# Kernel optimization log

Hardware: AMD Instinct MI355X
Metric: run time of the kernel (lower is better)

Reference implementation:

```python
import jax, jax.numpy as jnp
import numpy as np

NUM_NODES = 100000
NUM_EDGES = 600000
NUM_GRAPHS = 512
D = 128  # num_features == latent widths


def setup_inputs() -> dict:
    key = jax.random.key(0)
    ks = jax.random.split(key, 16)
    inp = {
        "x": jax.random.normal(ks[0], (NUM_NODES, D), dtype=jnp.float32),
        "edge_index": jax.random.randint(ks[1], (2, NUM_EDGES), 0, NUM_NODES, dtype=jnp.int32),
        "batch": jnp.sort(jax.random.randint(ks[2], (NUM_NODES,), 0, NUM_GRAPHS, dtype=jnp.int32)),
    }
    s = 1.0 / np.sqrt(D)
    # SAGEConv params per layer: lin_l (applied to mean-aggregated neighbors), lin_r (root), bias
    for i in range(3):
        inp[f"Wl{i+1}"] = jax.random.uniform(ks[3 + 3 * i], (D, D), jnp.float32, -s, s)
        inp[f"Wr{i+1}"] = jax.random.uniform(ks[4 + 3 * i], (D, D), jnp.float32, -s, s)
        inp[f"b{i+1}"] = jax.random.uniform(ks[5 + 3 * i], (D,), jnp.float32, -s, s)
    inp["Wro"] = jax.random.uniform(ks[12], (D, 1), jnp.float32, -s, s)
    inp["bro"] = jax.random.uniform(ks[13], (1,), jnp.float32, -s, s)
    return inp


def _sage_conv(h, Wl, Wr, b, src, dst):
    # mean aggregation of source features at destination nodes
    msg = jax.ops.segment_sum(h[src], dst, num_segments=NUM_NODES)          # [N, D]
    cnt = jax.ops.segment_sum(jnp.ones((src.shape[0], 1), h.dtype), dst,
                              num_segments=NUM_NODES)                        # [N, 1]
    mean = msg / jnp.maximum(cnt, 1.0)
    return mean @ Wl + h @ Wr + b


def reference(x, edge_index, batch, Wl1, Wr1, b1, Wl2, Wr2, b2, Wl3, Wr3, b3, Wro, bro):
    src, dst = edge_index[0], edge_index[1]
    h = x
    for Wl, Wr, b in ((Wl1, Wr1, b1), (Wl2, Wr2, b2), (Wl3, Wr3, b3)):
        h = jax.nn.relu(_sage_conv(h, Wl, Wr, b, src, dst))
    # per-graph sum pooling (replaces the python loop over unique batch ids)
    pooled = jax.ops.segment_sum(h, batch, num_segments=NUM_GRAPHS)  # [G, D]
    return jax.nn.sigmoid(pooled @ Wro + bro)  # [G, 1]
```

## Files before the change

### kernel.cpp

```cpp
#include <hip/hip_runtime.h>
#include <math.h>

#define N_NODES 100000
#define N_EDGES 600000
#define N_GRAPHS 512
#define D 128
#define SCAN_BS 1024
#define SCAN_NBC ((N_NODES + SCAN_BS - 1) / SCAN_BS)

typedef unsigned short u16;
typedef __attribute__((ext_vector_type(8))) short short8;
typedef __attribute__((ext_vector_type(4))) float f32x4;

__device__ __forceinline__ u16 f2bf(float f) {
    unsigned int u = __float_as_uint(f);
    u += 0x7FFFu + ((u >> 16) & 1u);
    return (u16)(u >> 16);
}
__device__ __forceinline__ float bf2f(u16 h) {
    return __uint_as_float(((unsigned int)h) << 16);
}
__device__ __forceinline__ void split2(float f, unsigned int& h16, unsigned int& l16) {
    unsigned int u = __float_as_uint(f);
    unsigned int hb = (u + (0x7FFFu + ((u >> 16) & 1u))) & 0xffff0000u;
    float lo = f - __uint_as_float(hb);
    unsigned int ul = __float_as_uint(lo);
    h16 = hb >> 16;
    l16 = (ul + (0x7FFFu + ((ul >> 16) & 1u))) >> 16;
}

typedef __attribute__((address_space(1))) const unsigned int gas_u32;
typedef __attribute__((address_space(3))) unsigned int las_u32;
__device__ __forceinline__ void gload16(const void* g, void* l) {
    __builtin_amdgcn_global_load_lds((gas_u32*)g, (las_u32*)l, 16, 0, 0);
}

__global__ __launch_bounds__(256) void zero_i_kernel(int* __restrict__ p, int n) {
    int i = blockIdx.x * 256 + threadIdx.x;
    if (i < n) p[i] = 0;
}

__global__ __launch_bounds__(256) void hist_kernel(const int* __restrict__ dst,
                                                   int* __restrict__ deg) {
    int e = blockIdx.x * 256 + threadIdx.x;
    if (e < N_EDGES) atomicAdd(&deg[dst[e]], 1);
}

__global__ __launch_bounds__(1024) void scan1_kernel(const int* __restrict__ deg,
                                                     int* __restrict__ excl,
                                                     int* __restrict__ blocksum) {
    __shared__ int buf[2][SCAN_BS];
    const int t = threadIdx.x;
    const int gid = blockIdx.x * SCAN_BS + t;
    int v = (gid < N_NODES) ? deg[gid] : 0;
    buf[0][t] = v;
    __syncthreads();
    int pi = 0;
    for (int off = 1; off < SCAN_BS; off <<= 1) {
        int val = buf[pi][t];
        if (t >= off) val += buf[pi][t - off];
        buf[pi ^ 1][t] = val;
        pi ^= 1;
        __syncthreads();
    }
    int incl = buf[pi][t];
    if (gid < N_NODES) excl[gid] = incl - v;
    if (t == SCAN_BS - 1) blocksum[blockIdx.x] = incl;
}

__global__ __launch_bounds__(256) void scan3_kernel(const int* __restrict__ excl,
                                                    const int* __restrict__ blocksum,
                                                    int* __restrict__ rowptr) {
    __shared__ int buf[2][128];
    const int t = threadIdx.x;
    if (t < 128) buf[0][t] = (t < SCAN_NBC) ? blocksum[t] : 0;
    __syncthreads();
    int pi = 0;
    for (int off = 1; off < 128; off <<= 1) {
        if (t < 128) {
            int val = buf[pi][t];
            if (t >= off) val += buf[pi][t - off];
            buf[pi ^ 1][t] = val;
        }
        pi ^= 1;
        __syncthreads();
    }
    const int i = blockIdx.x * 256 + t;
    if (i < N_NODES) {
        const int j = i / SCAN_BS;
        const int pref = (j == 0) ? 0 : buf[pi][j - 1];
        rowptr[i] = excl[i] + pref;
    }
    if (i == 0) rowptr[N_NODES] = N_EDGES;
}

__global__ __launch_bounds__(256) void fill_kernel(const int* __restrict__ src,
                                                   const int* __restrict__ dst,
                                                   const int* __restrict__ rowptr,
                                                   int* __restrict__ fill,
                                                   int* __restrict__ csr_src) {
    int e = blockIdx.x * 256 + threadIdx.x;
    if (e < N_EDGES) {
        int d = dst[e];
        int pos = rowptr[d] + atomicAdd(&fill[d], 1);
        csr_src[pos] = src[e];
    }
}

__global__ __launch_bounds__(256) void split_x_kernel(const float* __restrict__ x,
                                                      u16* __restrict__ Hhi,
                                                      u16* __restrict__ Hlo) {
    const int i = blockIdx.x * 256 + threadIdx.x;
    const float4 v = ((const float4*)x)[i];
    unsigned int h0, l0, h1, l1, h2, l2, h3, l3;
    split2(v.x, h0, l0); split2(v.y, h1, l1);
    split2(v.z, h2, l2); split2(v.w, h3, l3);
    uint2 oh, ol;
    oh.x = h0 | (h1 << 16); oh.y = h2 | (h3 << 16);
    ol.x = l0 | (l1 << 16); ol.y = l2 | (l3 << 16);
    ((uint2*)Hhi)[i] = oh;
    ((uint2*)Hlo)[i] = ol;
}

__global__ __launch_bounds__(64) void wprep_kernel(const float* __restrict__ Wl1, const float* __restrict__ Wr1,
                                                   const float* __restrict__ Wl2, const float* __restrict__ Wr2,
                                                   const float* __restrict__ Wl3, const float* __restrict__ Wr3,
                                                   u16* __restrict__ wph, u16* __restrict__ wpl) {
    const int layer = blockIdx.x >> 6;
    const int t = blockIdx.x & 63;
    const int lane = threadIdx.x;
    const float* Wl = (layer == 0) ? Wl1 : (layer == 1) ? Wl2 : Wl3;
    const float* Wr = (layer == 0) ? Wr1 : (layer == 1) ? Wr2 : Wr3;
    const int nt = t >> 3, kt = t & 7;
    const int n = nt * 16 + (lane & 15);
    const int k0 = kt * 32 + (lane >> 4) * 8;
    const size_t base = (size_t)layer * 32768 + (size_t)(t * 64 + lane) * 8;
    #pragma unroll
    for (int j = 0; j < 8; ++j) {
        const int k = k0 + j;
        const float w = (k < 128) ? Wl[k * 128 + n] : Wr[(k - 128) * 128 + n];
        const u16 h = f2bf(w);
        wph[base + j] = h;
        wpl[base + j] = f2bf(w - bf2f(h));
    }
}

__global__ __launch_bounds__(256) void agg_kernel(const u16* __restrict__ Hhi,
                                                  const int* __restrict__ rowptr,
                                                  const int* __restrict__ csr_src,
                                                  u16* __restrict__ Mb) {
    const int lane = threadIdx.x & 63;
    const int node = blockIdx.x * 4 + (threadIdx.x >> 6);
    if (node >= N_NODES) return;
    const int beg = rowptr[node];
    const int end = rowptr[node + 1];
    const unsigned int* H32 = (const unsigned int*)Hhi;
    float a0 = 0.f, a1 = 0.f;

    for (int c0 = beg; c0 < end; c0 += 64) {
        const int nv = min(64, end - c0);
        int msrc = (c0 + lane < end) ? csr_src[c0 + lane] : 0;
        int j = 0;
        for (; j + 4 <= nv; j += 4) {
            const int s0 = __shfl(msrc, j + 0);
            const int s1 = __shfl(msrc, j + 1);
            const int s2 = __shfl(msrc, j + 2);
            const int s3 = __shfl(msrc, j + 3);
            const unsigned int w0 = H32[(size_t)s0 * 64 + lane];
            const unsigned int w1 = H32[(size_t)s1 * 64 + lane];
            const unsigned int w2 = H32[(size_t)s2 * 64 + lane];
            const unsigned int w3 = H32[(size_t)s3 * 64 + lane];
            a0 += __uint_as_float(w0 << 16) + __uint_as_float(w1 << 16)
                + __uint_as_float(w2 << 16) + __uint_as_float(w3 << 16);
            a1 += __uint_as_float(w0 & 0xffff0000u) + __uint_as_float(w1 & 0xffff0000u)
                + __uint_as_float(w2 & 0xffff0000u) + __uint_as_float(w3 & 0xffff0000u);
        }
        for (; j < nv; ++j) {
            const int s = __shfl(msrc, j);
            const unsigned int w = H32[(size_t)s * 64 + lane];
            a0 += __uint_as_float(w << 16);
            a1 += __uint_as_float(w & 0xffff0000u);
        }
    }
    const float inv = 1.0f / (float)max(end - beg, 1);
    const unsigned int o = (unsigned int)f2bf(a0 * inv) | ((unsigned int)f2bf(a1 * inv) << 16);
    ((unsigned int*)Mb)[(size_t)node * 64 + lane] = o;
}

__global__ __launch_bounds__(512, 4) void gemm_kernel(const u16* __restrict__ Mb,
                                                      const u16* Hhi, const u16* Hlo,
                                                      const u16* __restrict__ Wph,
                                                      const u16* __restrict__ Wpl,
                                                      const float* __restrict__ bias,
                                                      u16* OHhi, u16* OHlo,
                                                      const float* __restrict__ Wro,
                                                      float* rowdot) {
    __shared__ uint4 ldsAll[5120];
    const int t = threadIdx.x;
    const int lane = t & 63;
    const int wv = t >> 6;
    const int m0 = blockIdx.x * 128 + wv * 16;
    int rm = m0 + (lane & 15);
    if (rm >= N_NODES) rm = 0;
    const int ko = (lane >> 4) * 8;

    short8 am[4], ah[4], al[4];
    #pragma unroll
    for (int kt = 0; kt < 4; ++kt) {
        am[kt] = *(const short8*)(Mb  + (size_t)rm * D + kt * 32 + ko);
        ah[kt] = *(const short8*)(Hhi + (size_t)rm * D + kt * 32 + ko);
        al[kt] = *(const short8*)(Hlo + (size_t)rm * D + kt * 32 + ko);
    }

    const int rowb = m0 + ((lane >> 4) << 2);
    const int cl = lane & 15;
    const int g4 = (lane >> 4) << 2;
    const u16* ldsU = (const u16*)ldsAll;
    char* bounceB = (char*)ldsAll + 65536 + wv * 2048;
    float wsum[4] = {0.f, 0.f, 0.f, 0.f};

    #pragma unroll
    for (int s = 0; s < 2; ++s) {
        if (s) __syncthreads();
        {
            const uint4* gh = (const uint4*)Wph + s * 2048;
            const uint4* gl = (const uint4*)Wpl + s * 2048;
            #pragma unroll
            for (int i = 0; i < 4; ++i) {
                gload16(gh + t + 512 * i, (void*)&ldsAll[wv * 64 + 512 * i]);
                gload16(gl + t + 512 * i, (void*)&ldsAll[2048 + wv * 64 + 512 * i]);
            }
        }
        __syncthreads();

        f32x4 acc4[4];
        #pragma unroll
        for (int nt2 = 0; nt2 < 4; ++nt2) {
            f32x4 acc = {0.f, 0.f, 0.f, 0.f};
            #pragma unroll
            for (int kt = 0; kt < 8; ++kt) {
                const int fo = (nt2 * 8 + kt) * 512 + lane * 8;
                const short8 bh = *(const short8*)(ldsU + fo);
                const short8 bl = *(const short8*)(ldsU + 16384 + fo);
                if (kt < 4) {
                    acc = __builtin_amdgcn_mfma_f32_16x16x32_bf16(am[kt], bh, acc, 0, 0, 0);
                    acc = __builtin_amdgcn_mfma_f32_16x16x32_bf16(am[kt], bl, acc, 0, 0, 0);
                } else {
                    acc = __builtin_amdgcn_mfma_f32_16x16x32_bf16(ah[kt - 4], bh, acc, 0, 0, 0);
                    acc = __builtin_amdgcn_mfma_f32_16x16x32_bf16(ah[kt - 4], bl, acc, 0, 0, 0);
                    acc = __builtin_amdgcn_mfma_f32_16x16x32_bf16(al[kt - 4], bh, acc, 0, 0, 0);
                }
            }
            acc4[nt2] = acc;
        }

        if (rowdot) {
            #pragma unroll
            for (int nt2 = 0; nt2 < 4; ++nt2) {
                const int col = (s * 4 + nt2) * 16 + cl;
                const float bv = bias[col];
                const float wroc = Wro[col];
                #pragma unroll
                for (int r = 0; r < 4; ++r) {
                    const float v = fmaxf(acc4[nt2][r] + bv, 0.f);
                    wsum[r] = fmaf(v, wroc, wsum[r]);
                }
            }
        } else {
            unsigned int lo_pack[8];
            #pragma unroll
            for (int nt2 = 0; nt2 < 4; ++nt2) {
                const int col = (s * 4 + nt2) * 16 + cl;
                const float bv = bias[col];
                #pragma unroll
                for (int r = 0; r < 4; ++r) {
                    const int row16 = g4 + r;
                    const float v = fmaxf(acc4[nt2][r] + bv, 0.f);
                    unsigned int h16, l16;
                    split2(v, h16, l16);
                    const int boff = (row16 * 128 + (nt2 * 16 + cl) * 2) ^ ((row16 & 7) << 4);
                    *(u16*)(bounceB + boff) = (u16)h16;
                    if (r & 1) lo_pack[nt2 * 2 + (r >> 1)] |= l16 << 16;
                    else       lo_pack[nt2 * 2 + (r >> 1)]  = l16;
                }
            }
            asm volatile("s_waitcnt lgkmcnt(0)" ::: "memory");
            #pragma unroll
            for (int j = 0; j < 2; ++j) {
                const int row16 = j * 8 + (lane >> 3);
                const int blk = lane & 7;
                const uint4 vv = *(const uint4*)(bounceB + row16 * 128 + ((blk ^ (row16 & 7)) << 4));
                const int grow = blockIdx.x * 128 + wv * 16 + row16;
                if (grow < N_NODES)
                    *(uint4*)(OHhi + (size_t)grow * D + s * 64 + blk * 8) = vv;
            }
            asm volatile("s_waitcnt lgkmcnt(0)" ::: "memory");
            #pragma unroll
            for (int nt2 = 0; nt2 < 4; ++nt2) {
                #pragma unroll
                for (int r = 0; r < 4; ++r) {
                    const int row16 = g4 + r;
                    const unsigned int l16 = (lo_pack[nt2 * 2 + (r >> 1)] >> ((r & 1) * 16)) & 0xffffu;
                    const int boff = (row16 * 128 + (nt2 * 16 + cl) * 2) ^ ((row16 & 7) << 4);
                    *(u16*)(bounceB + boff) = (u16)l16;
                }
            }
            asm volatile("s_waitcnt lgkmcnt(0)" ::: "memory");
            #pragma unroll
            for (int j = 0; j < 2; ++j) {
                const int row16 = j * 8 + (lane >> 3);
                const int blk = lane & 7;
                const uint4 vv = *(const uint4*)(bounceB + row16 * 128 + ((blk ^ (row16 & 7)) << 4));
                const int grow = blockIdx.x * 128 + wv * 16 + row16;
                if (grow < N_NODES)
                    *(uint4*)(OHlo + (size_t)grow * D + s * 64 + blk * 8) = vv;
            }
        }
    }

    if (rowdot) {
        #pragma unroll
        for (int r = 0; r < 4; ++r) {
            float tsum = wsum[r];
            tsum += __shfl_down(tsum, 8, 64);
            tsum += __shfl_down(tsum, 4, 64);
            tsum += __shfl_down(tsum, 2, 64);
            tsum += __shfl_down(tsum, 1, 64);
            const int row = rowb + r;
            if (cl == 0 && row < N_NODES) {
                rowdot[row] = tsum;
            }
        }
    }
}

__global__ __launch_bounds__(64) void final_kernel(const float* __restrict__ rowdot,
                                                   const int* __restrict__ batch,
                                                   const float* __restrict__ bro,
                                                   float* __restrict__ out) {
    const int g = blockIdx.x;
    const int t = threadIdx.x;
    int lo = 0, hi = N_NODES;
    while (lo < hi) { int mid = (lo + hi) >> 1; if (batch[mid] < g) lo = mid + 1; else hi = mid; }
    int lo2 = lo, hi2 = N_NODES;
    while (lo2 < hi2) { int mid = (lo2 + hi2) >> 1; if (batch[mid] < g + 1) lo2 = mid + 1; else hi2 = mid; }

    float acc = 0.0f;
    for (int i = lo + t; i < lo2; i += 64) acc += rowdot[i];
    #pragma unroll
    for (int off = 32; off > 0; off >>= 1) acc += __shfl_down(acc, off, 64);
    if (t == 0) out[g] = 1.0f / (1.0f + expf(-(acc + bro[0])));
}

extern "C" void kernel_launch(void* const* d_in, const int* in_sizes, int n_in,
                              void* d_out, int out_size, void* d_ws, size_t ws_size,
                              hipStream_t stream) {
    const float* x     = (const float*)d_in[0];
    const int*   ei    = (const int*)d_in[1];
    const int*   batch = (const int*)d_in[2];
    const int*   src   = ei;
    const int*   dst   = ei + N_EDGES;
    const float* Wl[3] = {(const float*)d_in[3], (const float*)d_in[6], (const float*)d_in[9]};
    const float* Wr[3] = {(const float*)d_in[4], (const float*)d_in[7], (const float*)d_in[10]};
    const float* bs[3] = {(const float*)d_in[5], (const float*)d_in[8], (const float*)d_in[11]};
    const float* Wro   = (const float*)d_in[12];
    const float* bro   = (const float*)d_in[13];
    float* out = (float*)d_out;

    const size_t ND = (size_t)N_NODES * D;
    char* ws = (char*)d_ws;
    u16* Hhi = (u16*)ws;
    u16* Hlo = Hhi + ND;
    u16* Mb  = Hlo + ND;
    u16* Wph = Mb + ND;
    u16* Wpl = Wph + 3 * 32768;
    int* deg      = (int*)(Wpl + 3 * 32768);
    int* fill     = deg + N_NODES;
    float* rowdot = (float*)(fill + N_NODES);
    int* excl     = (int*)(rowdot + N_NODES);
    int* blocksum = excl + N_NODES;
    int* rowptr   = blocksum + 128;
    int* csr_src  = rowptr + N_NODES + 1;

    const int EB      = (N_EDGES + 255) / 256;
    const int NB      = (N_NODES + 255) / 256;
    const int NB2     = (2 * N_NODES + 255) / 256;
    const int SPLIT_B = (int)(ND / 4 / 256);
    const int AGG_B   = N_NODES / 4;
    const int GEMM_B  = (N_NODES + 127) / 128;

    zero_i_kernel<<<NB2, 256, 0, stream>>>(deg, 2 * N_NODES);
    hist_kernel<<<EB, 256, 0, stream>>>(dst, deg);
    scan1_kernel<<<SCAN_NBC, SCAN_BS, 0, stream>>>(deg, excl, blocksum);
    scan3_kernel<<<NB, 256, 0, stream>>>(excl, blocksum, rowptr);
    fill_kernel<<<EB, 256, 0, stream>>>(src, dst, rowptr, fill, csr_src);

    split_x_kernel<<<SPLIT_B, 256, 0, stream>>>(x, Hhi, Hlo);
    wprep_kernel<<<192, 64, 0, stream>>>(Wl[0], Wr[0], Wl[1], Wr[1], Wl[2], Wr[2], Wph, Wpl);

    for (int l = 0; l < 3; ++l) {
        float* rdl = (l == 2) ? rowdot : (float*)nullptr;
        agg_kernel<<<AGG_B, 256, 0, stream>>>(Hhi, rowptr, csr_src, Mb);
        gemm_kernel<<<GEMM_B, 512, 0, stream>>>(Mb, Hhi, Hlo,
                                                Wph + l * 32768, Wpl + l * 32768, bs[l],
                                                Hhi, Hlo, Wro, rdl);
    }

    final_kernel<<<N_GRAPHS, 64, 0, stream>>>(rowdot, batch, bro, out);
}
```

Measured before the change: 406.3 us.

## Double-buffer weight staging in SAGE GEMM and unroll neighbor gather by eight

The GEMM kernel now stages the weight matrix in four quarter-chunks across two LDS buffers. It waits with partial vmcnt so the next chunk's global-to-LDS load overlaps the current chunk's MFMA work, where before it loaded halves and synchronised in between. The epilogue is moved after all compute, which needs eight accumulator vectors to stay live and raises register pressure. The aggregation loop also gets an 8-wide unroll so more gather loads are in flight per wave.

```diff
diff --git a/kernel.cpp b/kernel.cpp
--- a/kernel.cpp
+++ b/kernel.cpp
@@ -161,6 +161,32 @@
         const int nv = min(64, end - c0);
         int msrc = (c0 + lane < end) ? csr_src[c0 + lane] : 0;
         int j = 0;
+        for (; j + 8 <= nv; j += 8) {
+            const int s0 = __shfl(msrc, j + 0);
+            const int s1 = __shfl(msrc, j + 1);
+            const int s2 = __shfl(msrc, j + 2);
+            const int s3 = __shfl(msrc, j + 3);
+            const int s4 = __shfl(msrc, j + 4);
+            const int s5 = __shfl(msrc, j + 5);
+            const int s6 = __shfl(msrc, j + 6);
+            const int s7 = __shfl(msrc, j + 7);
+            const unsigned int w0 = H32[(size_t)s0 * 64 + lane];
+            const unsigned int w1 = H32[(size_t)s1 * 64 + lane];
+            const unsigned int w2 = H32[(size_t)s2 * 64 + lane];
+            const unsigned int w3 = H32[(size_t)s3 * 64 + lane];
+            const unsigned int w4 = H32[(size_t)s4 * 64 + lane];
+            const unsigned int w5 = H32[(size_t)s5 * 64 + lane];
+            const unsigned int w6 = H32[(size_t)s6 * 64 + lane];
+            const unsigned int w7 = H32[(size_t)s7 * 64 + lane];
+            a0 += __uint_as_float(w0 << 16) + __uint_as_float(w1 << 16)
+                + __uint_as_float(w2 << 16) + __uint_as_float(w3 << 16)
+                + __uint_as_float(w4 << 16) + __uint_as_float(w5 << 16)
+                + __uint_as_float(w6 << 16) + __uint_as_float(w7 << 16);
+            a1 += __uint_as_float(w0 & 0xffff0000u) + __uint_as_float(w1 & 0xffff0000u)
+                + __uint_as_float(w2 & 0xffff0000u) + __uint_as_float(w3 & 0xffff0000u)
+                + __uint_as_float(w4 & 0xffff0000u) + __uint_as_float(w5 & 0xffff0000u)
+                + __uint_as_float(w6 & 0xffff0000u) + __uint_as_float(w7 & 0xffff0000u);
+        }
         for (; j + 4 <= nv; j += 4) {
             const int s0 = __shfl(msrc, j + 0);
             const int s1 = __shfl(msrc, j + 1);
@@ -212,70 +238,108 @@
         al[kt] = *(const short8*)(Hlo + (size_t)rm * D + kt * 32 + ko);
     }
 
-    const int rowb = m0 + ((lane >> 4) << 2);
     const int cl = lane & 15;
     const int g4 = (lane >> 4) << 2;
-    const u16* ldsU = (const u16*)ldsAll;
     char* bounceB = (char*)ldsAll + 65536 + wv * 2048;
-    float wsum[4] = {0.f, 0.f, 0.f, 0.f};
-
-    #pragma unroll
-    for (int s = 0; s < 2; ++s) {
-        if (s) __syncthreads();
-        {
-            const uint4* gh = (const uint4*)Wph + s * 2048;
-            const uint4* gl = (const uint4*)Wpl + s * 2048;
-            #pragma unroll
-            for (int i = 0; i < 4; ++i) {
-                gload16(gh + t + 512 * i, (void*)&ldsAll[wv * 64 + 512 * i]);
-                gload16(gl + t + 512 * i, (void*)&ldsAll[2048 + wv * 64 + 512 * i]);
-            }
-        }
-        __syncthreads();
-
-        f32x4 acc4[4];
+
+    f32x4 acc8[2][4];
+
+#define STAGE_W(Q, B) do {                                                      \
+        const uint4* gh_ = (const uint4*)Wph + (Q) * 1024;                      \
+        const uint4* gl_ = (const uint4*)Wpl + (Q) * 1024;                      \
+        _Pragma("unroll")                                                       \
+        for (int i_ = 0; i_ < 2; ++i_) {                                        \
+            gload16(gh_ + t + 512 * i_,                                         \
+                    (void*)&ldsAll[(B) * 2048 + wv * 64 + 512 * i_]);           \
+            gload16(gl_ + t + 512 * i_,                                         \
+                    (void*)&ldsAll[(B) * 2048 + 1024 + wv * 64 + 512 * i_]);    \
+        }                                                                       \
+    } while (0)
+
+#define COMPUTE_S(Q, B) do {                                                    \
+        const u16* bufU_ = (const u16*)(ldsAll + (B) * 2048);                   \
+        _Pragma("unroll")                                                       \
+        for (int l_ = 0; l_ < 2; ++l_) {                                        \
+            f32x4 acc_ = {0.f, 0.f, 0.f, 0.f};                                  \
+            _Pragma("unroll")                                                   \
+            for (int kt_ = 0; kt_ < 8; ++kt_) {                                 \
+                const int fo_ = (l_ * 8 + kt_) * 512 + lane * 8;                \
+                const short8 bh_ = *(const short8*)(bufU_ + fo_);               \
+                const short8 bl_ = *(const short8*)(bufU_ + 8192 + fo_);        \
+                if (kt_ < 4) {                                                  \
+                    acc_ = __builtin_amdgcn_mfma_f32_16x16x32_bf16(am[kt_], bh_, acc_, 0, 0, 0); \
+                    acc_ = __builtin_amdgcn_mfma_f32_16x16x32_bf16(am[kt_], bl_, acc_, 0, 0, 0); \
+                } else {                                                        \
+                    acc_ = __builtin_amdgcn_mfma_f32_16x16x32_bf16(ah[kt_ - 4], bh_, acc_, 0, 0, 0); \
+                    acc_ = __builtin_amdgcn_mfma_f32_16x16x32_bf16(ah[kt_ - 4], bl_, acc_, 0, 0, 0); \
+                    acc_ = __builtin_amdgcn_mfma_f32_16x16x32_bf16(al[kt_ - 4], bh_, acc_, 0, 0, 0); \
+                }                                                               \
+            }                                                                   \
+            acc8[(Q) >> 1][((Q) & 1) * 2 + l_] = acc_;                          \
+        }                                                                       \
+    } while (0)
+
+    STAGE_W(0, 0);
+    __builtin_amdgcn_sched_barrier(0);
+    STAGE_W(1, 1);
+    asm volatile("s_waitcnt vmcnt(4)" ::: "memory");
+    __builtin_amdgcn_s_barrier();
+    COMPUTE_S(0, 0);
+    __builtin_amdgcn_s_barrier();
+    STAGE_W(2, 0);
+    asm volatile("s_waitcnt vmcnt(4)" ::: "memory");
+    __builtin_amdgcn_s_barrier();
+    COMPUTE_S(1, 1);
+    __builtin_amdgcn_s_barrier();
+    STAGE_W(3, 1);
+    asm volatile("s_waitcnt vmcnt(4)" ::: "memory");
+    __builtin_amdgcn_s_barrier();
+    COMPUTE_S(2, 0);
+    asm volatile("s_waitcnt vmcnt(0)" ::: "memory");
+    __builtin_amdgcn_s_barrier();
+    COMPUTE_S(3, 1);
+
+    if (rowdot) {
+        float wsum[4] = {0.f, 0.f, 0.f, 0.f};
         #pragma unroll
-        for (int nt2 = 0; nt2 < 4; ++nt2) {
-            f32x4 acc = {0.f, 0.f, 0.f, 0.f};
-            #pragma unroll
-            for (int kt = 0; kt < 8; ++kt) {
-                const int fo = (nt2 * 8 + kt) * 512 + lane * 8;
-                const short8 bh = *(const short8*)(ldsU + fo);
-                const short8 bl = *(const short8*)(ldsU + 16384 + fo);
-                if (kt < 4) {
-                    acc = __builtin_amdgcn_mfma_f32_16x16x32_bf16(am[kt], bh, acc, 0, 0, 0);
-                    acc = __builtin_amdgcn_mfma_f32_16x16x32_bf16(am[kt], bl, acc, 0, 0, 0);
-                } else {
-                    acc = __builtin_amdgcn_mfma_f32_16x16x32_bf16(ah[kt - 4], bh, acc, 0, 0, 0);
-                    acc = __builtin_amdgcn_mfma_f32_16x16x32_bf16(ah[kt - 4], bl, acc, 0, 0, 0);
-                    acc = __builtin_amdgcn_mfma_f32_16x16x32_bf16(al[kt - 4], bh, acc, 0, 0, 0);
-                }
-            }
-            acc4[nt2] = acc;
-        }
-
-        if (rowdot) {
+        for (int si = 0; si < 2; ++si) {
             #pragma unroll
             for (int nt2 = 0; nt2 < 4; ++nt2) {
-                const int col = (s * 4 + nt2) * 16 + cl;
+                const int col = (si * 4 + nt2) * 16 + cl;
                 const float bv = bias[col];
                 const float wroc = Wro[col];
                 #pragma unroll
                 for (int r = 0; r < 4; ++r) {
-                    const float v = fmaxf(acc4[nt2][r] + bv, 0.f);
+                    const float v = fmaxf(acc8[si][nt2][r] + bv, 0.f);
                     wsum[r] = fmaf(v, wroc, wsum[r]);
                 }
             }
-        } else {
+        }
+        #pragma unroll
+        for (int r = 0; r < 4; ++r) {
+            float tsum = wsum[r];
+            tsum += __shfl_down(tsum, 8, 64);
+            tsum += __shfl_down(tsum, 4, 64);
+            tsum += __shfl_down(tsum, 2, 64);
+            tsum += __shfl_down(tsum, 1, 64);
+            const int row = m0 + g4 + r;
+            if (cl == 0 && row < N_NODES) {
+                rowdot[row] = tsum;
+            }
+        }
+    } else {
+        #pragma unroll
+        for (int si = 0; si < 2; ++si) {
+            asm volatile("s_waitcnt lgkmcnt(0)" ::: "memory");
             unsigned int lo_pack[8];
             #pragma unroll
             for (int nt2 = 0; nt2 < 4; ++nt2) {
-                const int col = (s * 4 + nt2) * 16 + cl;
+                const int col = (si * 4 + nt2) * 16 + cl;
                 const float bv = bias[col];
                 #pragma unroll
                 for (int r = 0; r < 4; ++r) {
                     const int row16 = g4 + r;
-                    const float v = fmaxf(acc4[nt2][r] + bv, 0.f);
+                    const float v = fmaxf(acc8[si][nt2][r] + bv, 0.f);
                     unsigned int h16, l16;
                     split2(v, h16, l16);
                     const int boff = (row16 * 128 + (nt2 * 16 + cl) * 2) ^ ((row16 & 7) << 4);
@@ -292,7 +356,7 @@
                 const uint4 vv = *(const uint4*)(bounceB + row16 * 128 + ((blk ^ (row16 & 7)) << 4));
                 const int grow = blockIdx.x * 128 + wv * 16 + row16;
                 if (grow < N_NODES)
-                    *(uint4*)(OHhi + (size_t)grow * D + s * 64 + blk * 8) = vv;
+                    *(uint4*)(OHhi + (size_t)grow * D + si * 64 + blk * 8) = vv;
             }
             asm volatile("s_waitcnt lgkmcnt(0)" ::: "memory");
             #pragma unroll
@@ -313,25 +377,12 @@
                 const uint4 vv = *(const uint4*)(bounceB + row16 * 128 + ((blk ^ (row16 & 7)) << 4));
                 const int grow = blockIdx.x * 128 + wv * 16 + row16;
                 if (grow < N_NODES)
-                    *(uint4*)(OHlo + (size_t)grow * D + s * 64 + blk * 8) = vv;
-            }
-        }
-    }
-
-    if (rowdot) {
-        #pragma unroll
-        for (int r = 0; r < 4; ++r) {
-            float tsum = wsum[r];
-            tsum += __shfl_down(tsum, 8, 64);
-            tsum += __shfl_down(tsum, 4, 64);
-            tsum += __shfl_down(tsum, 2, 64);
-            tsum += __shfl_down(tsum, 1, 64);
-            const int row = rowb + r;
-            if (cl == 0 && row < N_NODES) {
-                rowdot[row] = tsum;
-            }
-        }
-    }
+                    *(uint4*)(OHlo + (size_t)grow * D + si * 64 + blk * 8) = vv;
+            }
+        }
+    }
+#undef STAGE_W
+#undef COMPUTE_S
 }
 
 __global__ __launch_bounds__(64) void final_kernel(const float* __restrict__ rowdot,
```

Measured after the change: 388.3 us. -4.4%, faster.
